# Kernel optimization log

Hardware: AMD Instinct MI355X
Metric: run time of the kernel (lower is better)

The kernel has to match this reference:

```python
import jax, jax.numpy as jnp
import numpy as np

B = 16384
D_SUP, D_ANOM, D_IND = 1024, 128, 2048
D_IN = D_SUP + D_ANOM + D_IND  # 3200
H1, FEAT = 256, 128
DEPTH = 12            # hologram_depth
N_COND = 14           # num_conditions
CAP = 256             # hologram_capacity
INTERFERENCE_STRENGTH = 0.42
NUM_SPECTRA = 8
SPECTRAL_BOOST = 1.0 + 0.1 * NUM_SPECTRA  # 1.8


def setup_inputs() -> dict:
    key = jax.random.key(0)
    ks = jax.random.split(key, 16)
    s = lambda k, shape, scale=1.0: jax.random.normal(k, shape, dtype=jnp.float32) * scale
    inp = {
        "superposition": s(ks[0], (B, D_SUP)),
        "anomaly": s(ks[1], (B, D_ANOM)),
        "individual": s(ks[2], (B, D_IND)),
        # interference_processor: Linear(3200,256) -> ReLU -> Linear(256,128) -> ReLU
        "ip_W1": s(ks[3], (D_IN, H1), 1.0 / np.sqrt(D_IN)),
        "ip_b1": jnp.zeros((H1,), jnp.float32),
        "ip_W2": s(ks[4], (H1, FEAT), 1.0 / np.sqrt(H1)),
        "ip_b2": jnp.zeros((FEAT,), jnp.float32),
        "cons_W": s(ks[5], (DEPTH, FEAT, FEAT), 1.0 / np.sqrt(FEAT)),
        "cons_b": jnp.zeros((DEPTH, FEAT), jnp.float32),
        # 14 memory banks
        "ref_patterns": s(ks[6], (N_COND, CAP, FEAT)),
        "obj_patterns": s(ks[7], (N_COND, CAP, FEAT)),
        "ret_W": s(ks[8], (N_COND, FEAT, FEAT), 1.0 / np.sqrt(FEAT)),
        "ret_b": jnp.zeros((N_COND, FEAT), jnp.float32),
    }
    return inp


def reference(superposition, anomaly, individual, ip_W1, ip_b1, ip_W2, ip_b2,
              cons_W, cons_b, ref_patterns, obj_patterns, ret_W, ret_b):
    # combined input [B, 3200]
    x = jnp.concatenate([superposition, anomaly, individual], axis=1)
    # interference processor (dropout is identity in eval)
    h = jax.nn.relu(x @ ip_W1 + ip_b1)
    h = jax.nn.relu(h @ ip_W2 + ip_b2)  # [B, 128]

    # 12-layer memory consolidator via scan
    def step(state, wb):
        w, b = wb
        return jax.nn.relu(state @ w + b), None
    memory_state, _ = jax.lax.scan(step, h, (cons_W, cons_b))  # [B, 128]

    # All 14 banks batched: similarities [B, K, C]
    ref_sim = jnp.einsum('bd,kcd->bkc', memory_state, ref_patterns)
    obj_sim = jnp.einsum('bd,kcd->bkc', memory_state, obj_patterns)
    interference = ref_sim * obj_sim * (INTERFERENCE_STRENGTH * SPECTRAL_BOOST)

    # retrieval networks: [B, K, 128]
    retrieved = jnp.einsum('bd,kde->bke', memory_state, ret_W) + ret_b[None, :, :]

    anomaly_weight = jnp.mean(jnp.abs(anomaly), axis=1, keepdims=True)  # [B, 1]
    interference_weight = jnp.mean(interference, axis=2)                # [B, K]
    combined_weight = interference_weight + 0.3 * anomaly_weight        # [B, K]

    return retrieved * combined_weight[:, :, None]  # [B, 14, 128]
```

## Files before the change

### kernel.cpp

```cpp
#include <hip/hip_runtime.h>
#include <stdint.h>


typedef __attribute__((ext_vector_type(4))) float f32x4;
typedef __attribute__((ext_vector_type(8))) short s16x8;

#define SCALE_IW 0.002953125f

__device__ __forceinline__ ushort f2bf(float f) {
  uint32_t u = __builtin_bit_cast(uint32_t, f);
  u += 0x7fffu + ((u >> 16) & 1u);
  return (ushort)(u >> 16);
}
__device__ __forceinline__ float bf2f(ushort u) {
  return __builtin_bit_cast(float, ((uint32_t)u) << 16);
}
__device__ __forceinline__ uint pack2(float a, float b) {
  return (uint)f2bf(a) | ((uint)f2bf(b) << 16);
}
__device__ __forceinline__ void gl_lds16(const ushort* g, ushort* l) {
  __builtin_amdgcn_global_load_lds(
      (const __attribute__((address_space(1))) uint32_t*)g,
      (__attribute__((address_space(3))) uint32_t*)l, 16, 0, 0);
}
__device__ __forceinline__ f32x4 mfma16(s16x8 a, s16x8 b, f32x4 c) {
  return __builtin_amdgcn_mfma_f32_16x16x32_bf16(a, b, c, 0, 0, 0);
}

#define BARRIER_LGKM()                                                      \
  do {                                                                      \
    asm volatile("s_waitcnt lgkmcnt(0)" ::: "memory");                      \
    __builtin_amdgcn_s_barrier();                                           \
    asm volatile("" ::: "memory");                                          \
  } while (0)

__global__ __launch_bounds__(256) void k_prep_w1(const float* __restrict__ w1,
                                                 ushort* __restrict__ w1s) {
  const int ks = blockIdx.x, ch = blockIdx.y, t = threadIdx.x;
  ushort* out = w1s + ((size_t)ch * 100 + ks) * 4096;
#pragma unroll
  for (int i = 0; i < 2; ++i) {
    const int p = i * 256 + t, c = p >> 7, n = p & 127;
    float v[8];
#pragma unroll
    for (int j = 0; j < 8; ++j)
      v[j] = w1[(size_t)(ks * 32 + c * 8 + j) * 256 + ch * 128 + n];
    uint4 o;
    o.x = pack2(v[0], v[1]);
    o.y = pack2(v[2], v[3]);
    o.z = pack2(v[4], v[5]);
    o.w = pack2(v[6], v[7]);
    *(uint4*)(out + (size_t)(c * 128 + n) * 8) = o;
  }
}

__global__ __launch_bounds__(256) void k_prep_nk(const float* __restrict__ in,
                                                 ushort* __restrict__ out,
                                                 int in_slice, int out_slice) {
  const int t = threadIdx.x;
  const float* src = in + (size_t)blockIdx.y * in_slice;
  ushort* dst = out + (size_t)blockIdx.y * out_slice;
  const int cg = blockIdx.x * 2 + (t >> 7), n = t & 127;
  float v[8];
#pragma unroll
  for (int j = 0; j < 8; ++j) v[j] = src[(size_t)(cg * 8 + j) * 128 + n];
  uint4 o;
  o.x = pack2(v[0], v[1]);
  o.y = pack2(v[2], v[3]);
  o.z = pack2(v[4], v[5]);
  o.w = pack2(v[6], v[7]);
  *(uint4*)(dst + (size_t)cg * 1024 + n * 8) = o;
}

__global__ __launch_bounds__(128) void k_build_mt(const float* __restrict__ ref,
                                                  const float* __restrict__ obj,
                                                  ushort* __restrict__ ms) {
  const int k = blockIdx.y, e0 = blockIdx.x * 8, d = threadIdx.x;
  const float* rp = ref + (size_t)k * 256 * 128;
  const float* op = obj + (size_t)k * 256 * 128;
  float acc[8] = {};
  for (int c = 0; c < 256; ++c) {
    const float rv = rp[c * 128 + d];
#pragma unroll
    for (int j = 0; j < 8; ++j) acc[j] += rv * op[c * 128 + e0 + j];
  }
  ushort* o = ms + (size_t)k * 16384 + (d >> 3) * 1024 + (d & 7);
#pragma unroll
  for (int j = 0; j < 8; ++j) o[(e0 + j) * 8] = f2bf(acc[j] * SCALE_IW);
}

__global__ __launch_bounds__(256, 8) void k_gemm1(
    const float* __restrict__ sup, const float* __restrict__ anom,
    const float* __restrict__ ind, const ushort* __restrict__ w1s,
    const float* __restrict__ b1, ushort* __restrict__ h1) {
  __shared__ alignas(16) ushort As[2][16 * 40];
  __shared__ alignas(16) ushort Bs[2][4096];
  const int t = threadIdx.x;
  const int w = t >> 6, l = t & 63, m = l & 15, q = l >> 4;
  const int n0 = blockIdx.x * 128;
  const int b0 = blockIdx.y * 16;
  const int ar = t >> 4, ac = t & 15;
  const ushort* wbase = w1s + (size_t)blockIdx.x * 409600;
  f32x4 acc[2] = {};
  float2 xr;

#define XLOAD(KS)                                                         \
  {                                                                       \
    const int k0_ = (KS) * 32;                                            \
    const float* src_;                                                    \
    int rs_, ko_;                                                         \
    if (k0_ < 1024)      { src_ = sup;  rs_ = 1024; ko_ = k0_; }          \
    else if (k0_ < 1152) { src_ = anom; rs_ = 128;  ko_ = k0_ - 1024; }   \
    else                 { src_ = ind;  rs_ = 2048; ko_ = k0_ - 1152; }   \
    xr = *(const float2*)(src_ + (size_t)(b0 + ar) * rs_ + ko_ + ac * 2); \
  }
#define STAGE_A(BUF) \
  { *(uint*)(As[BUF] + ar * 40 + ac * 2) = pack2(xr.x, xr.y); }
#define STAGE_B(KS, BUF)                                       \
  {                                                            \
    _Pragma("unroll")                                          \
    for (int i_ = 0; i_ < 2; ++i_) {                           \
      const int s_ = i_ * 256 + t;                             \
      gl_lds16(wbase + (size_t)(KS) * 4096 + s_ * 8,           \
               Bs[BUF] + s_ * 8);                              \
    }                                                          \
  }

  XLOAD(0);
  STAGE_A(0);
  STAGE_B(0, 0);
  XLOAD(1);
  for (int ks = 0; ks < 100; ++ks) {
    __syncthreads();
    const int cur = ks & 1, nxt = cur ^ 1;
    if (ks < 99) {
      STAGE_A(nxt);
      STAGE_B(ks + 1, nxt);
      if (ks < 98) XLOAD(ks + 2);
    }
    const s16x8 af = *(const s16x8*)(As[cur] + m * 40 + q * 8);
#pragma unroll
    for (int ct = 0; ct < 2; ++ct) {
      const s16x8 bf =
          *(const s16x8*)(Bs[cur] + q * 1024 + (w * 32 + ct * 16 + m) * 8);
      acc[ct] = mfma16(af, bf, acc[ct]);
    }
  }
#undef XLOAD
#undef STAGE_A
#undef STAGE_B
#pragma unroll
  for (int ct = 0; ct < 2; ++ct) {
    const int col = n0 + w * 32 + ct * 16 + m;
    const float bias = b1[col];
#pragma unroll
    for (int r = 0; r < 4; ++r) {
      const int row = b0 + q * 4 + r;
      h1[(size_t)row * 256 + col] = f2bf(fmaxf(acc[ct][r] + bias, 0.f));
    }
  }
}

__global__ __launch_bounds__(256, 2) void k_cons(
    const ushort* __restrict__ h1, const ushort* __restrict__ w2s,
    const ushort* __restrict__ cws, const float* __restrict__ b2,
    const float* __restrict__ cb, ushort* __restrict__ stateg) {
  __shared__ alignas(16) ushort A0[32 * 264];
  __shared__ alignas(16) ushort S0[32 * 136];
  __shared__ alignas(16) ushort S1[32 * 136];
  __shared__ alignas(16) ushort Wh[2][8192];
  const int t = threadIdx.x;
  const int w = t >> 6, l = t & 63, m = l & 15, q = l >> 4;
  const int b0 = blockIdx.x * 32;

  auto stage = [&](int p) {
    const ushort* src = (p < 4) ? w2s + (size_t)p * 8192
                                : cws + (size_t)(p - 4) * 8192;
    ushort* dst = Wh[p & 1];
#pragma unroll
    for (int i = 0; i < 4; ++i) {
      const int s = i * 256 + t;
      gl_lds16(src + s * 8, dst + s * 8);
    }
  };

  stage(0);
#pragma unroll
  for (int i = 0; i < 4; ++i) {
    const int s = i * 256 + t, r = s >> 5, c = s & 31;
    *(uint4*)(A0 + r * 264 + c * 8) =
        *(const uint4*)(h1 + (size_t)(b0 + r) * 256 + c * 8);
  }

  f32x4 acc[2][2] = {};
  for (int p = 0; p < 28; ++p) {
    __syncthreads();
    if (p < 27) stage(p + 1);
    const int layer = (p < 4) ? 0 : 1 + ((p - 4) >> 1);
    const ushort* Asrc;
    int astr, koff;
    if (p < 4) { Asrc = A0; astr = 264; koff = p * 64; }
    else {
      Asrc = (layer & 1) ? (const ushort*)S0 : (const ushort*)S1;
      astr = 136;
      koff = ((p - 4) & 1) * 64;
    }
    const ushort* Wb = Wh[p & 1];
#pragma unroll
    for (int ksl = 0; ksl < 2; ++ksl) {
      const int cl = ksl * 4 + q;
      s16x8 af[2];
#pragma unroll
      for (int rt = 0; rt < 2; ++rt)
        af[rt] = *(const s16x8*)(Asrc + (rt * 16 + m) * astr + koff + cl * 8);
#pragma unroll
      for (int ct = 0; ct < 2; ++ct) {
        const s16x8 bf =
            *(const s16x8*)(Wb + cl * 1024 + (w * 32 + ct * 16 + m) * 8);
#pragma unroll
        for (int rt = 0; rt < 2; ++rt)
          acc[rt][ct] = mfma16(af[rt], bf, acc[rt][ct]);
      }
    }
    const bool layer_end = (p == 3) || (p >= 4 && ((p - 4) & 1));
    if (layer_end) {
      const float* bias = (layer == 0) ? b2 : cb + (layer - 1) * 128;
      ushort* dst = (layer & 1) ? S1 : S0;
#pragma unroll
      for (int ct = 0; ct < 2; ++ct) {
        const int col = w * 32 + ct * 16 + m;
        const float bv = bias[col];
#pragma unroll
        for (int rt = 0; rt < 2; ++rt)
#pragma unroll
          for (int r = 0; r < 4; ++r) {
            dst[(rt * 16 + q * 4 + r) * 136 + col] =
                f2bf(fmaxf(acc[rt][ct][r] + bv, 0.f));
            acc[rt][ct][r] = 0.f;
          }
      }
    }
  }
  __syncthreads();
  const ushort* fin = S0;
#pragma unroll
  for (int i = 0; i < 2; ++i) {
    const int s = i * 256 + t, r = s >> 4, c = s & 15;
    *(uint4*)(stateg + (size_t)(b0 + r) * 128 + c * 8) =
        *(const uint4*)(fin + r * 136 + c * 8);
  }
}

__global__ __launch_bounds__(256, 2) void k_banks(
    const ushort* __restrict__ stateg, const float* __restrict__ anom,
    const ushort* __restrict__ ms, const ushort* __restrict__ rws,
    const float* __restrict__ retb, float* __restrict__ out) {
  __shared__ alignas(16) ushort S[32 * 136];
  __shared__ alignas(16) ushort Mb[16384];
  __shared__ alignas(16) ushort Rb[16384];
  __shared__ alignas(16) float iwbuf[4][32];
  __shared__ alignas(16) float wvs[32];
  __shared__ alignas(16) float aws[32];
  const int t = threadIdx.x;
  const int w = t >> 6, l = t & 63, m = l & 15, q = l >> 4;
  const int b0 = blockIdx.x * 32;

  auto stagek = [&](int kk) {
#pragma unroll
    for (int i = 0; i < 8; ++i) {
      const int s = i * 256 + t;
      gl_lds16(ms + (size_t)kk * 16384 + s * 8, Mb + s * 8);
      gl_lds16(rws + (size_t)kk * 16384 + s * 8, Rb + s * 8);
    }
  };

  stagek(0);
#pragma unroll
  for (int i = 0; i < 2; ++i) {
    const int s = i * 256 + t, r = s >> 4, c = s & 15;
    *(uint4*)(S + r * 136 + c * 8) =
        *(const uint4*)(stateg + (size_t)(b0 + r) * 128 + c * 8);
  }
  {
    const int r = t >> 3, qq = t & 7;
    float sa = 0.f;
#pragma unroll
    for (int j = 0; j < 4; ++j) {
      const float4 v =
          *(const float4*)(anom + (size_t)(b0 + r) * 128 + qq * 16 + j * 4);
      sa += fabsf(v.x) + fabsf(v.y) + fabsf(v.z) + fabsf(v.w);
    }
    sa += __shfl_xor(sa, 1, 8);
    sa += __shfl_xor(sa, 2, 8);
    sa += __shfl_xor(sa, 4, 8);
    if (qq == 0) aws[r] = sa * (0.3f / 128.f);
  }
  __syncthreads();
  s16x8 af[4][2];
#pragma unroll
  for (int ks = 0; ks < 4; ++ks)
#pragma unroll
    for (int rt = 0; rt < 2; ++rt)
      af[ks][rt] = *(const s16x8*)(S + (rt * 16 + m) * 136 + (ks * 4 + q) * 8);
  float sc[2][4][2];
#pragma unroll
  for (int rt = 0; rt < 2; ++rt)
#pragma unroll
    for (int r = 0; r < 4; ++r)
#pragma unroll
      for (int ct = 0; ct < 2; ++ct)
        sc[rt][r][ct] =
            bf2f(S[(rt * 16 + q * 4 + r) * 136 + (w * 32 + ct * 16 + m)]);

  for (int k = 0; k < 14; ++k) {
    __syncthreads();
    f32x4 P[2][2] = {}, R[2][2] = {};
#pragma unroll
    for (int ks = 0; ks < 4; ++ks)
#pragma unroll
      for (int ct = 0; ct < 2; ++ct) {
        const int boff = (ks * 4 + q) * 1024 + (w * 32 + ct * 16 + m) * 8;
        const s16x8 bm = *(const s16x8*)(Mb + boff);
        const s16x8 br = *(const s16x8*)(Rb + boff);
#pragma unroll
        for (int rt = 0; rt < 2; ++rt) {
          P[rt][ct] = mfma16(af[ks][rt], bm, P[rt][ct]);
          R[rt][ct] = mfma16(af[ks][rt], br, R[rt][ct]);
        }
      }
#pragma unroll
    for (int rt = 0; rt < 2; ++rt) {
      float pr[4];
#pragma unroll
      for (int r = 0; r < 4; ++r) {
        float v = P[rt][0][r] * sc[rt][r][0] + P[rt][1][r] * sc[rt][r][1];
        v += __shfl_xor(v, 1, 16);
        v += __shfl_xor(v, 2, 16);
        v += __shfl_xor(v, 4, 16);
        v += __shfl_xor(v, 8, 16);
        pr[r] = v;
      }
      if (m == 0)
        *(float4*)&iwbuf[w][rt * 16 + q * 4] =
            make_float4(pr[0], pr[1], pr[2], pr[3]);
    }
    BARRIER_LGKM();
    if (k < 13) stagek(k + 1);
    if (t < 32)
      wvs[t] = iwbuf[0][t] + iwbuf[1][t] + iwbuf[2][t] + iwbuf[3][t] + aws[t];
    BARRIER_LGKM();
#pragma unroll
    for (int ct = 0; ct < 2; ++ct) {
      const int col = w * 32 + ct * 16 + m;
      const float rb = retb[k * 128 + col];
#pragma unroll
      for (int rt = 0; rt < 2; ++rt) {
        const float4 wv4 = *(const float4*)&wvs[rt * 16 + q * 4];
        const float wvv[4] = {wv4.x, wv4.y, wv4.z, wv4.w};
#pragma unroll
        for (int r = 0; r < 4; ++r) {
          const int row = b0 + rt * 16 + q * 4 + r;
          out[(size_t)row * 1792 + k * 128 + col] = wvv[r] * (R[rt][ct][r] + rb);
        }
      }
    }
  }
}

extern "C" void kernel_launch(void* const* d_in, const int* in_sizes, int n_in,
                              void* d_out, int out_size, void* d_ws,
                              size_t ws_size, hipStream_t stream) {
  const float* sup   = (const float*)d_in[0];
  const float* anom  = (const float*)d_in[1];
  const float* ind   = (const float*)d_in[2];
  const float* ipW1  = (const float*)d_in[3];
  const float* ipb1  = (const float*)d_in[4];
  const float* ipW2  = (const float*)d_in[5];
  const float* ipb2  = (const float*)d_in[6];
  const float* consW = (const float*)d_in[7];
  const float* consb = (const float*)d_in[8];
  const float* refp  = (const float*)d_in[9];
  const float* objp  = (const float*)d_in[10];
  const float* retW  = (const float*)d_in[11];
  const float* retb  = (const float*)d_in[12];
  float* out = (float*)d_out;
  char* ws = (char*)d_ws;
  ushort* W1S = (ushort*)(ws);
  ushort* W2S = (ushort*)(ws + 1638400);
  ushort* CWS = (ushort*)(ws + 1703936);
  ushort* RWS = (ushort*)(ws + 2097152);
  ushort* MS  = (ushort*)(ws + 2555904);
  ushort* H1  = (ushort*)(ws + 3014656);
  ushort* ST  = (ushort*)(ws + 11403264);

  k_prep_w1<<<dim3(100, 2), 256, 0, stream>>>(ipW1, W1S);
  k_prep_nk<<<dim3(16, 1), 256, 0, stream>>>(ipW2, W2S, 0, 0);
  k_prep_nk<<<dim3(8, 12), 256, 0, stream>>>(consW, CWS, 16384, 16384);
  k_prep_nk<<<dim3(8, 14), 256, 0, stream>>>(retW, RWS, 16384, 16384);
  k_build_mt<<<dim3(16, 14), 128, 0, stream>>>(refp, objp, MS);
  k_gemm1<<<dim3(2, 1024), 256, 0, stream>>>(sup, anom, ind, W1S, ipb1, H1);
  k_cons<<<512, 256, 0, stream>>>(H1, W2S, CWS, ipb2, consb, ST);
  k_banks<<<512, 256, 0, stream>>>(ST, anom, MS, RWS, retb, out);
}
```

Baseline: 495.4 us.

## Double gemm1 row tile and prefetch eight K-steps of activations ahead

After: 434.2 us. 12.3% less time.

```diff
diff --git a/kernel.cpp b/kernel.cpp
--- a/kernel.cpp
+++ b/kernel.cpp
@@ -89,22 +89,22 @@
   for (int j = 0; j < 8; ++j) o[(e0 + j) * 8] = f2bf(acc[j] * SCALE_IW);
 }
 
-__global__ __launch_bounds__(256, 8) void k_gemm1(
+__global__ __launch_bounds__(256, 4) void k_gemm1(
     const float* __restrict__ sup, const float* __restrict__ anom,
     const float* __restrict__ ind, const ushort* __restrict__ w1s,
     const float* __restrict__ b1, ushort* __restrict__ h1) {
-  __shared__ alignas(16) ushort As[2][16 * 40];
+  __shared__ alignas(16) ushort As[2][32 * 40];
   __shared__ alignas(16) ushort Bs[2][4096];
   const int t = threadIdx.x;
   const int w = t >> 6, l = t & 63, m = l & 15, q = l >> 4;
   const int n0 = blockIdx.x * 128;
-  const int b0 = blockIdx.y * 16;
-  const int ar = t >> 4, ac = t & 15;
+  const int b0 = blockIdx.y * 32;
+  const int ar = t >> 3, ac = t & 7;
   const ushort* wbase = w1s + (size_t)blockIdx.x * 409600;
-  f32x4 acc[2] = {};
-  float2 xr;
-
-#define XLOAD(KS)                                                         \
+  f32x4 acc[2][2] = {};
+  float4 xr[8];
+
+#define XLOAD(KS, SLOT)                                                   \
   {                                                                       \
     const int k0_ = (KS) * 32;                                            \
     const float* src_;                                                    \
@@ -112,10 +112,16 @@
     if (k0_ < 1024)      { src_ = sup;  rs_ = 1024; ko_ = k0_; }          \
     else if (k0_ < 1152) { src_ = anom; rs_ = 128;  ko_ = k0_ - 1024; }   \
     else                 { src_ = ind;  rs_ = 2048; ko_ = k0_ - 1152; }   \
-    xr = *(const float2*)(src_ + (size_t)(b0 + ar) * rs_ + ko_ + ac * 2); \
-  }
-#define STAGE_A(BUF) \
-  { *(uint*)(As[BUF] + ar * 40 + ac * 2) = pack2(xr.x, xr.y); }
+    xr[SLOT] =                                                            \
+        *(const float4*)(src_ + (size_t)(b0 + ar) * rs_ + ko_ + ac * 4);  \
+  }
+#define STAGE_A(BUF, SLOT)                                    \
+  {                                                           \
+    uint2 pk_;                                                \
+    pk_.x = pack2(xr[SLOT].x, xr[SLOT].y);                    \
+    pk_.y = pack2(xr[SLOT].z, xr[SLOT].w);                    \
+    *(uint2*)(As[BUF] + ar * 40 + ac * 4) = pk_;              \
+  }
 #define STAGE_B(KS, BUF)                                       \
   {                                                            \
     _Pragma("unroll")                                          \
@@ -125,39 +131,75 @@
                Bs[BUF] + s_ * 8);                              \
     }                                                          \
   }
-
-  XLOAD(0);
-  STAGE_A(0);
+#define COMPUTE(CUR)                                                        \
+  {                                                                         \
+    s16x8 af_[2], bf_[2];                                                   \
+    _Pragma("unroll")                                                       \
+    for (int rt = 0; rt < 2; ++rt)                                          \
+      af_[rt] = *(const s16x8*)(As[CUR] + (rt * 16 + m) * 40 + q * 8);      \
+    _Pragma("unroll")                                                       \
+    for (int ct = 0; ct < 2; ++ct)                                          \
+      bf_[ct] =                                                             \
+          *(const s16x8*)(Bs[CUR] + q * 1024 + (w * 32 + ct * 16 + m) * 8); \
+    _Pragma("unroll")                                                       \
+    for (int rt = 0; rt < 2; ++rt)                                          \
+      _Pragma("unroll")                                                     \
+      for (int ct = 0; ct < 2; ++ct)                                        \
+        acc[rt][ct] = mfma16(af_[rt], bf_[ct], acc[rt][ct]);                \
+  }
+
+  XLOAD(0, 0);
+  STAGE_A(0, 0);
   STAGE_B(0, 0);
-  XLOAD(1);
-  for (int ks = 0; ks < 100; ++ks) {
-    __syncthreads();
-    const int cur = ks & 1, nxt = cur ^ 1;
-    if (ks < 99) {
-      STAGE_A(nxt);
+  XLOAD(1, 1);
+
+  for (int g = 0; g < 12; ++g) {
+    const int g8 = g * 8;
+#pragma unroll
+    for (int u = 0; u < 8; ++u) {
+      const int ks = g8 + u;
+      __syncthreads();
+      const int cur = u & 1, nxt = cur ^ 1;
+      STAGE_A(nxt, (u + 1) & 7);
       STAGE_B(ks + 1, nxt);
-      if (ks < 98) XLOAD(ks + 2);
-    }
-    const s16x8 af = *(const s16x8*)(As[cur] + m * 40 + q * 8);
-#pragma unroll
-    for (int ct = 0; ct < 2; ++ct) {
-      const s16x8 bf =
-          *(const s16x8*)(Bs[cur] + q * 1024 + (w * 32 + ct * 16 + m) * 8);
-      acc[ct] = mfma16(af, bf, acc[ct]);
-    }
-  }
+      if (u == 0) {
+#pragma unroll
+        for (int j = 0; j < 8; ++j) XLOAD(g8 + 2 + j, (2 + j) & 7);
+      }
+      COMPUTE(cur);
+    }
+  }
+  __syncthreads();
+  STAGE_A(1, 1);
+  STAGE_B(97, 1);
+  XLOAD(98, 2);
+  XLOAD(99, 3);
+  COMPUTE(0);
+  __syncthreads();
+  STAGE_A(0, 2);
+  STAGE_B(98, 0);
+  COMPUTE(1);
+  __syncthreads();
+  STAGE_A(1, 3);
+  STAGE_B(99, 1);
+  COMPUTE(0);
+  __syncthreads();
+  COMPUTE(1);
 #undef XLOAD
 #undef STAGE_A
 #undef STAGE_B
+#undef COMPUTE
 #pragma unroll
   for (int ct = 0; ct < 2; ++ct) {
     const int col = n0 + w * 32 + ct * 16 + m;
     const float bias = b1[col];
 #pragma unroll
-    for (int r = 0; r < 4; ++r) {
-      const int row = b0 + q * 4 + r;
-      h1[(size_t)row * 256 + col] = f2bf(fmaxf(acc[ct][r] + bias, 0.f));
-    }
+    for (int rt = 0; rt < 2; ++rt)
+#pragma unroll
+      for (int r = 0; r < 4; ++r) {
+        const int row = b0 + rt * 16 + q * 4 + r;
+        h1[(size_t)row * 256 + col] = f2bf(fmaxf(acc[rt][ct][r] + bias, 0.f));
+      }
   }
 }
 
@@ -398,7 +440,7 @@
   k_prep_nk<<<dim3(8, 12), 256, 0, stream>>>(consW, CWS, 16384, 16384);
   k_prep_nk<<<dim3(8, 14), 256, 0, stream>>>(retW, RWS, 16384, 16384);
   k_build_mt<<<dim3(16, 14), 128, 0, stream>>>(refp, objp, MS);
-  k_gemm1<<<dim3(2, 1024), 256, 0, stream>>>(sup, anom, ind, W1S, ipb1, H1);
+  k_gemm1<<<dim3(2, 512), 256, 0, stream>>>(sup, anom, ind, W1S, ipb1, H1);
   k_cons<<<512, 256, 0, stream>>>(H1, W2S, CWS, ipb2, consb, ST);
   k_banks<<<512, 256, 0, stream>>>(ST, anom, MS, RWS, retb, out);
 }
```
